# Kernel optimization log

Hardware: AMD Instinct MI355X
Metric: run time of the kernel (lower is better)

## Reference

```python
import jax, jax.numpy as jnp
import numpy as np

EPS = 1e-5
NEG_SLOPE = 0.2


def batchnorm_nodes(x, gamma, beta):
    # BatchNorm2d over channel=node axis; x: [N, T, D], stats over (T, D) per node
    m = x.mean(axis=(1, 2), keepdims=True)
    v = ((x - m) ** 2).mean(axis=(1, 2), keepdims=True)
    return (x - m) * jax.lax.rsqrt(v + EPS) * gamma[:, None, None] + beta[:, None, None]


def gat_relation(h, src, dst, W, al, ar, N):
    # h: [N, T, D]; W: [D, H, dh]; al/ar: [H, dh]
    z = jnp.einsum('ntd,dhe->nthe', h, W)              # [N, T, H, dh]
    el = jnp.einsum('nthe,he->nth', z, al)             # [N, T, H]
    er = jnp.einsum('nthe,he->nth', z, ar)
    e = jax.nn.leaky_relu(el[src] + er[dst], NEG_SLOPE)  # [E, T, H]
    emax = jax.ops.segment_max(e, dst, num_segments=N)   # [N, T, H]
    ex = jnp.exp(e - emax[dst])
    denom = jax.ops.segment_sum(ex, dst, num_segments=N)
    alpha = ex / jnp.maximum(denom[dst], 1e-16)          # segment softmax over in-edges
    msg = alpha[..., None] * z[src]                      # [E, T, H, dh]
    return jax.ops.segment_sum(msg, dst, num_segments=N)  # [N, T, H, dh]


def setup_inputs() -> dict:
    key = jax.random.key(0)
    ks = jax.random.split(key, 12)
    N, T, D, H, E, DFF = 10000, 12, 64, 4, 100000, 128
    dh = D // H
    s = 0.1
    return {
        'x': jax.random.normal(ks[0], (N, T, D), jnp.float32),
        'src1': jax.random.randint(ks[1], (E,), 0, N, jnp.int32),
        'dst1': jax.random.randint(ks[2], (E,), 0, N, jnp.int32),
        'src2': jax.random.randint(ks[3], (E,), 0, N, jnp.int32),
        'dst2': jax.random.randint(ks[4], (E,), 0, N, jnp.int32),
        'W1': jax.random.normal(ks[5], (D, H, dh), jnp.float32) * s,
        'al1': jax.random.normal(ks[6], (H, dh), jnp.float32) * s,
        'ar1': jax.random.normal(ks[7], (H, dh), jnp.float32) * s,
        'W2': jax.random.normal(ks[8], (D, H, dh), jnp.float32) * s,
        'al2': jax.random.normal(ks[9], (H, dh), jnp.float32) * s,
        'ar2': jax.random.normal(ks[10], (H, dh), jnp.float32) * s,
        'bn1_g': jnp.ones((N,), jnp.float32),
        'bn1_b': jnp.zeros((N,), jnp.float32),
        'bn2_g': jnp.ones((N,), jnp.float32),
        'bn2_b': jnp.zeros((N,), jnp.float32),
        'ff_w1': jax.random.normal(ks[11], (D, DFF), jnp.float32) * s,
        'ff_b1': jnp.zeros((DFF,), jnp.float32),
        'ff_w2': jax.random.normal(jax.random.fold_in(key, 99), (DFF, D), jnp.float32) * s,
        'ff_b2': jnp.zeros((D,), jnp.float32),
    }


def reference(x, src1, dst1, src2, dst2, W1, al1, ar1, W2, al2, ar2,
              bn1_g, bn1_b, bn2_g, bn2_b, ff_w1, ff_b1, ff_w2, ff_b2):
    N, T, D = x.shape
    h = batchnorm_nodes(x, bn1_g, bn1_b)
    # HeteroGraphConv: per-relation GAT, sum aggregation
    m = gat_relation(h, src1, dst1, W1, al1, ar1, N) \
      + gat_relation(h, src2, dst2, W2, al2, ar2, N)   # [N, T, H, dh]
    m = m.reshape(N, T, D)
    x2 = x + m                                          # residual (dropout=identity in eval)
    h2 = batchnorm_nodes(x2, bn2_g, bn2_b)
    ff = jax.nn.gelu(h2 @ ff_w1 + ff_b1, approximate=False) @ ff_w2 + ff_b2
    return x2 + ff
```

## Files before the change

kernel.cpp:

```cpp
#include <hip/hip_runtime.h>
#include <math.h>

constexpr int kT = 12;
constexpr float kNeg = 0.2f;
constexpr float kEps = 1e-5f;
constexpr float kLog2e = 1.44269504088896f;

typedef __attribute__((ext_vector_type(8))) short bf16x8;
typedef __attribute__((ext_vector_type(4))) float f32x4;
typedef __attribute__((ext_vector_type(2))) float f32x2;

__device__ __forceinline__ short f2bf(float f) {
  union { float f; unsigned u; } v;
  v.f = f;
  return (short)((v.u + 0x7fffu + ((v.u >> 16) & 1u)) >> 16);
}
__device__ __forceinline__ unsigned pack2(float a, float b) {
  return (unsigned)(unsigned short)f2bf(a) | ((unsigned)(unsigned short)f2bf(b) << 16);
}

__device__ __forceinline__ float wave_reduce_sum(float v) {
#pragma unroll
  for (int o = 32; o > 0; o >>= 1) v += __shfl_xor(v, o);
  return v;
}

template <int CTRL>
__device__ __forceinline__ float qperm(float v) {
  int i = __float_as_int(v);
  return __int_as_float(__builtin_amdgcn_update_dpp(i, i, CTRL, 0xf, 0xf, false));
}

__global__ void prep_kernel(const float* __restrict__ x, const float* __restrict__ g,
                            const float* __restrict__ b, float* __restrict__ scale,
                            float* __restrict__ shift, const float* __restrict__ fw1,
                            const float* __restrict__ fw2, const float* __restrict__ zW1,
                            const float* __restrict__ zW2, const float* __restrict__ al1,
                            const float* __restrict__ ar1, const float* __restrict__ al2,
                            const float* __restrict__ ar2, bf16x8* __restrict__ fw1f,
                            bf16x8* __restrict__ fw2f, bf16x8* __restrict__ zw1f,
                            bf16x8* __restrict__ zw2f, bf16x8* __restrict__ walf,
                            const int* __restrict__ dst1, const int* __restrict__ dst2,
                            int* __restrict__ deg1, int* __restrict__ deg2, int N, int E1,
                            int E2, int nBnBlk) {
  int blk = blockIdx.x;
  int lane = threadIdx.x & 63, wid = threadIdx.x >> 6;
  if (blk < nBnBlk) {
    int n = blk * 4 + wid;
    if (n < N) {
      const float* xr = x + (size_t)n * 768;
      float s = 0.f, s2 = 0.f;
#pragma unroll
      for (int c = 0; c < 3; c++) {
        float4 v = *(const float4*)&xr[c * 256 + lane * 4];
        s += v.x + v.y + v.z + v.w;
        s2 += v.x * v.x + v.y * v.y + v.z * v.z + v.w * v.w;
      }
      s = wave_reduce_sum(s);
      s2 = wave_reduce_sum(s2);
      if (lane == 0) {
        const float inv = 1.f / 768.f;
        float mean = s * inv;
        float var = s2 * inv - mean * mean;
        float sc = rsqrtf(var + kEps) * g[n];
        scale[n] = sc;
        shift[n] = b[n] - mean * sc;
      }
    }
    return;
  }
  blk -= nBnBlk;
  int m = lane & 15, q = lane >> 4;
  if (blk == 0) {
    for (int fi = wid; fi < 16; fi += 4) {
      int mt = fi >> 1, kc = fi & 1;
      bf16x8 v;
#pragma unroll
      for (int j = 0; j < 8; j++) v[j] = f2bf(fw1[(kc * 32 + q * 8 + j) * 128 + mt * 16 + m]);
      fw1f[fi * 64 + lane] = v;
    }
    return;
  }
  if (blk == 1) {
    for (int fi = wid; fi < 16; fi += 4) {
      int mt2 = fi >> 2, kc2 = fi & 3;
      bf16x8 u;
#pragma unroll
      for (int j = 0; j < 8; j++) u[j] = f2bf(fw2[(kc2 * 32 + q * 8 + j) * 64 + mt2 * 16 + m]);
      fw2f[fi * 64 + lane] = u;
    }
    return;
  }
  if (blk == 2) {
    for (int fi = wid; fi < 8; fi += 4) {
      int mt = fi >> 1, kc = fi & 1;
      bf16x8 v, u;
#pragma unroll
      for (int j = 0; j < 8; j++) {
        int d = kc * 32 + q * 8 + j;
        v[j] = f2bf(zW1[d * 64 + mt * 16 + m]);
        u[j] = f2bf(zW2[d * 64 + mt * 16 + m]);
      }
      zw1f[fi * 64 + lane] = v;
      zw2f[fi * 64 + lane] = u;
    }
    return;
  }
  if (blk == 3) {
    __shared__ float wal[16][64];
    for (int e0 = threadIdx.x; e0 < 1024; e0 += 256) {
      int f = e0 >> 6, d = e0 & 63;
      int h = f & 3;
      const float* av = (f < 4) ? al1 : (f < 8) ? ar1 : (f < 12) ? al2 : ar2;
      const float* W = (f < 8) ? zW1 : zW2;
      float s = 0.f;
#pragma unroll
      for (int e = 0; e < 16; e++) s += W[d * 64 + h * 16 + e] * av[h * 16 + e];
      wal[f][d] = s * kLog2e;
    }
    __syncthreads();
    if (wid == 0) {
#pragma unroll
      for (int kc = 0; kc < 2; kc++) {
        bf16x8 v;
#pragma unroll
        for (int j = 0; j < 8; j++) v[j] = f2bf(wal[m][kc * 32 + q * 8 + j]);
        walf[kc * 64 + lane] = v;
      }
    }
    return;
  }
  int i = (blk - 4) * 256 + threadIdx.x;
  if (i < E1) atomicAdd(&deg1[dst1[i]], 1);
  else if (i < E1 + E2) atomicAdd(&deg2[dst2[i - E1]], 1);
}

__global__ void scan_kernel(const int* __restrict__ deg1, int* __restrict__ off1,
                            const int* __restrict__ deg2, int* __restrict__ off2, int N) {
  const int* deg = blockIdx.x ? deg2 : deg1;
  int* off = blockIdx.x ? off2 : off1;
  __shared__ int wsum[16];
  __shared__ int carry;
  int tid = threadIdx.x, lane = tid & 63, wv = tid >> 6;
  if (tid == 0) { carry = 0; off[0] = 0; }
  __syncthreads();
  for (int base = 0; base < N; base += 1024) {
    int i = base + tid;
    int incl = (i < N) ? deg[i] : 0;
#pragma unroll
    for (int o = 1; o < 64; o <<= 1) {
      int y = __shfl_up(incl, o);
      if (lane >= o) incl += y;
    }
    if (lane == 63) wsum[wv] = incl;
    __syncthreads();
    if (tid < 16) {
      int p = wsum[tid];
#pragma unroll
      for (int o = 1; o < 16; o <<= 1) {
        int y = __shfl_up(p, o);
        if (tid >= o) p += y;
      }
      wsum[tid] = p;
    }
    __syncthreads();
    int prefix = carry + (wv > 0 ? wsum[wv - 1] : 0);
    if (i < N) off[i + 1] = prefix + incl;
    int total = carry + wsum[15];
    __syncthreads();
    if (tid == 0) carry = total;
    __syncthreads();
  }
}

__global__ __launch_bounds__(256) void fillzel_kernel(
    const int* __restrict__ src1, const int* __restrict__ dst1, const int* __restrict__ off1,
    int* __restrict__ cur1, int* __restrict__ scsr1, const int* __restrict__ src2,
    const int* __restrict__ dst2, const int* __restrict__ off2, int* __restrict__ cur2,
    int* __restrict__ scsr2, int E1, int E2, int nZelBlk,
    const float* __restrict__ x, const float* __restrict__ scale,
    const float* __restrict__ shift, const bf16x8* __restrict__ zw1f,
    const bf16x8* __restrict__ zw2f, const bf16x8* __restrict__ walf,
    unsigned short* __restrict__ z1, unsigned short* __restrict__ z2,
    float* __restrict__ el1, float* __restrict__ er1, float* __restrict__ el2,
    float* __restrict__ er2, int NT) {
  if ((int)blockIdx.x >= nZelBlk) {
    int i = ((int)blockIdx.x - nZelBlk) * 256 + threadIdx.x;
    if (i < E1) {
      int d = dst1[i];
      int p = atomicAdd(&cur1[d], 1);
      scsr1[off1[d] + p] = src1[i] * kT;
    } else if (i < E1 + E2) {
      int k = i - E1;
      int d = dst2[k];
      int p = atomicAdd(&cur2[d], 1);
      scsr2[off2[d] + p] = src2[k] * kT;
    }
    return;
  }
  __shared__ bf16x8 sW1[8][64];
  __shared__ bf16x8 sW2[8][64];
  __shared__ bf16x8 sWE[2][64];
  int lane = threadIdx.x & 63, wid = threadIdx.x >> 6;
  int m = lane & 15, q = lane >> 4;
  for (int fi = wid; fi < 8; fi += 4) {
    sW1[fi][lane] = zw1f[fi * 64 + lane];
    sW2[fi][lane] = zw2f[fi * 64 + lane];
  }
  if (wid == 0) {
    sWE[0][lane] = walf[lane];
    sWE[1][lane] = walf[64 + lane];
  }
  __syncthreads();
  int ntile = (NT + 15) / 16;
  for (int tile = blockIdx.x * 4 + wid; tile < ntile; tile += nZelBlk * 4) {
    int r0 = tile * 16;
    int row = r0 + m;
    int rowc = (row < NT) ? row : NT - 1;
    int n = rowc / kT;
    float sc = scale[n], sh = shift[n];
    bf16x8 hf[2];
#pragma unroll
    for (int kc = 0; kc < 2; kc++) {
      float4 p0 = *(const float4*)&x[(size_t)rowc * 64 + kc * 32 + q * 8];
      float4 p1 = *(const float4*)&x[(size_t)rowc * 64 + kc * 32 + q * 8 + 4];
      hf[kc][0] = f2bf(fmaf(p0.x, sc, sh));
      hf[kc][1] = f2bf(fmaf(p0.y, sc, sh));
      hf[kc][2] = f2bf(fmaf(p0.z, sc, sh));
      hf[kc][3] = f2bf(fmaf(p0.w, sc, sh));
      hf[kc][4] = f2bf(fmaf(p1.x, sc, sh));
      hf[kc][5] = f2bf(fmaf(p1.y, sc, sh));
      hf[kc][6] = f2bf(fmaf(p1.z, sc, sh));
      hf[kc][7] = f2bf(fmaf(p1.w, sc, sh));
    }
    f32x4 a1[4], a2[4], ae;
#pragma unroll
    for (int mt = 0; mt < 4; mt++) {
      a1[mt] = (f32x4){0.f, 0.f, 0.f, 0.f};
      a2[mt] = (f32x4){0.f, 0.f, 0.f, 0.f};
    }
    ae = (f32x4){0.f, 0.f, 0.f, 0.f};
#pragma unroll
    for (int kc = 0; kc < 2; kc++) {
#pragma unroll
      for (int mt = 0; mt < 4; mt++) {
        a1[mt] = __builtin_amdgcn_mfma_f32_16x16x32_bf16(sW1[mt * 2 + kc][lane], hf[kc],
                                                         a1[mt], 0, 0, 0);
        a2[mt] = __builtin_amdgcn_mfma_f32_16x16x32_bf16(sW2[mt * 2 + kc][lane], hf[kc],
                                                         a2[mt], 0, 0, 0);
      }
      ae = __builtin_amdgcn_mfma_f32_16x16x32_bf16(sWE[kc][lane], hf[kc], ae, 0, 0, 0);
    }
    if (row < NT) {
      float* edst = (q == 0) ? el1 : (q == 1) ? er1 : (q == 2) ? el2 : er2;
      *(float4*)&edst[(size_t)row * 4] = make_float4(ae[0], ae[1], ae[2], ae[3]);
#pragma unroll
      for (int mt = 0; mt < 4; mt++) {
        uint2 u1 = {pack2(a1[mt][0], a1[mt][1]), pack2(a1[mt][2], a1[mt][3])};
        uint2 u2 = {pack2(a2[mt][0], a2[mt][1]), pack2(a2[mt][2], a2[mt][3])};
        *(uint2*)&z1[(size_t)row * 64 + mt * 16 + 4 * q] = u1;
        *(uint2*)&z2[(size_t)row * 64 + mt * 16 + 4 * q] = u2;
      }
    }
  }
}

struct GBuf {
  uint2 z0, z1, z2, z3;
  float e;
};

__device__ __forceinline__ void pf_group(int sbl, int eb, int t, int zvoff,
                                         const float* __restrict__ elp,
                                         const unsigned short* __restrict__ zp, int qidx,
                                         GBuf& G) {
  int sg = __shfl(sbl, eb + qidx) + t;
  G.e = elp[(size_t)sg * 4];
  int s0 = __builtin_amdgcn_readlane(sbl, eb);
  int s1 = __builtin_amdgcn_readlane(sbl, eb + 1);
  int s2 = __builtin_amdgcn_readlane(sbl, eb + 2);
  int s3 = __builtin_amdgcn_readlane(sbl, eb + 3);
  G.z0 = *(const uint2*)(zp + (size_t)s0 * 64 + zvoff);
  G.z1 = *(const uint2*)(zp + (size_t)s1 * 64 + zvoff);
  G.z2 = *(const uint2*)(zp + (size_t)s2 * 64 + zvoff);
  G.z3 = *(const uint2*)(zp + (size_t)s3 * 64 + zvoff);
}

__device__ __forceinline__ void cg_group(const GBuf& G, float er_h, int rem, int qidx,
                                         float& den, f32x2& n01, f32x2& n23) {
  float ev = G.e + er_h;
  ev = fmaxf(ev, kNeg * ev);
  float w = exp2f(ev);
  w = (qidx < rem) ? w : 0.f;
  den += w;
  float w0 = qperm<0x00>(w);
  float w1 = qperm<0x55>(w);
  float w2 = qperm<0xAA>(w);
  float w3 = qperm<0xFF>(w);
  f32x2 v;
  v = (f32x2){__uint_as_float(G.z0.x << 16), __uint_as_float(G.z0.x & 0xffff0000u)};
  n01 += v * w0;
  v = (f32x2){__uint_as_float(G.z0.y << 16), __uint_as_float(G.z0.y & 0xffff0000u)};
  n23 += v * w0;
  v = (f32x2){__uint_as_float(G.z1.x << 16), __uint_as_float(G.z1.x & 0xffff0000u)};
  n01 += v * w1;
  v = (f32x2){__uint_as_float(G.z1.y << 16), __uint_as_float(G.z1.y & 0xffff0000u)};
  n23 += v * w1;
  v = (f32x2){__uint_as_float(G.z2.x << 16), __uint_as_float(G.z2.x & 0xffff0000u)};
  n01 += v * w2;
  v = (f32x2){__uint_as_float(G.z2.y << 16), __uint_as_float(G.z2.y & 0xffff0000u)};
  n23 += v * w2;
  v = (f32x2){__uint_as_float(G.z3.x << 16), __uint_as_float(G.z3.x & 0xffff0000u)};
  n01 += v * w3;
  v = (f32x2){__uint_as_float(G.z3.y << 16), __uint_as_float(G.z3.y & 0xffff0000u)};
  n23 += v * w3;
}

__device__ __forceinline__ void gat_rel(int n, int t, int zvoff, const int* __restrict__ scsr,
                                        const int* __restrict__ off,
                                        const float* __restrict__ elp, float er_h,
                                        const unsigned short* __restrict__ zp, int lane,
                                        int qidx, f32x2& a01, f32x2& a23) {
  int b0 = off[n], b1 = off[n + 1];
  if (b1 <= b0) return;
  float den = 0.f;
  f32x2 n01 = {0.f, 0.f}, n23 = {0.f, 0.f};
  for (int c0 = b0; c0 < b1; c0 += 64) {
    int cnt = b1 - c0;
    if (cnt > 64) cnt = 64;
    int idx = c0 + lane;
    int sbl = scsr[(idx < b1) ? idx : b1 - 1];
    GBuf A, B, C, D;
    pf_group(sbl, 0, t, zvoff, elp, zp, qidx, A);
    if (cnt > 4) pf_group(sbl, 4, t, zvoff, elp, zp, qidx, B);
    if (cnt > 8) pf_group(sbl, 8, t, zvoff, elp, zp, qidx, C);
    int g = 0;
    while (true) {
      if (g + 12 < cnt) pf_group(sbl, g + 12, t, zvoff, elp, zp, qidx, D);
      cg_group(A, er_h, cnt - g, qidx, den, n01, n23);
      g += 4;
      if (g >= cnt) break;
      if (g + 12 < cnt) pf_group(sbl, g + 12, t, zvoff, elp, zp, qidx, A);
      cg_group(B, er_h, cnt - g, qidx, den, n01, n23);
      g += 4;
      if (g >= cnt) break;
      if (g + 12 < cnt) pf_group(sbl, g + 12, t, zvoff, elp, zp, qidx, B);
      cg_group(C, er_h, cnt - g, qidx, den, n01, n23);
      g += 4;
      if (g >= cnt) break;
      if (g + 12 < cnt) pf_group(sbl, g + 12, t, zvoff, elp, zp, qidx, C);
      cg_group(D, er_h, cnt - g, qidx, den, n01, n23);
      g += 4;
      if (g >= cnt) break;
    }
  }
  den += qperm<0xB1>(den);
  den += qperm<0x4E>(den);
  float inv = 1.f / den;
  a01 += n01 * inv;
  a23 += n23 * inv;
}

__global__ __launch_bounds__(256) void agg_kernel(
    const float* __restrict__ x, const int* __restrict__ scsr1,
    const int* __restrict__ off1, const float* __restrict__ el1,
    const float* __restrict__ er1, const unsigned short* __restrict__ z1,
    const int* __restrict__ scsr2, const int* __restrict__ off2,
    const float* __restrict__ el2, const float* __restrict__ er2,
    const unsigned short* __restrict__ z2, float* __restrict__ x2,
    float* __restrict__ bn2s, float* __restrict__ bn2q, int N) {
  int wid = threadIdx.x >> 6, lane = threadIdx.x & 63;
  int w = blockIdx.x * 4 + wid;
  if (w >= N * 3) return;
  int n = w / 3;
  int t0 = (w - n * 3) * 4;
  int tl = lane >> 4, cg = lane & 15;
  int t = t0 + tl;
  int row = n * kT + t;
  int h = cg >> 2;
  int qidx = lane & 3;
  int zvoff = t * 64 + cg * 4;
  f32x2 a01 = {0.f, 0.f}, a23 = {0.f, 0.f};
  gat_rel(n, t, zvoff, scsr1, off1, el1 + h, er1[(size_t)row * 4 + h], z1, lane, qidx, a01,
          a23);
  gat_rel(n, t, zvoff, scsr2, off2, el2 + h, er2[(size_t)row * 4 + h], z2, lane, qidx, a01,
          a23);

  size_t base = (size_t)row * 64 + cg * 4;
  float4 xr = *(const float4*)&x[base];
  float4 o;
  o.x = xr.x + a01.x;
  o.y = xr.y + a01.y;
  o.z = xr.z + a23.x;
  o.w = xr.w + a23.y;
  *(float4*)&x2[base] = o;
  float s1 = o.x + o.y + o.z + o.w;
  float s2 = o.x * o.x + o.y * o.y + o.z * o.z + o.w * o.w;
  s1 = wave_reduce_sum(s1);
  s2 = wave_reduce_sum(s2);
  if (lane == 0) {
    atomicAdd(&bn2s[n], s1);
    atomicAdd(&bn2q[n], s2);
  }
}

__global__ __launch_bounds__(256, 2) void ff_kernel(
    const float* __restrict__ x2, const float* __restrict__ bn2s,
    const float* __restrict__ bn2q, const float* __restrict__ bng,
    const float* __restrict__ bnb, const bf16x8* __restrict__ w1f,
    const bf16x8* __restrict__ w2f, const float* __restrict__ b1,
    const float* __restrict__ b2, float* __restrict__ out, int NT) {
  __shared__ bf16x8 sW1[16][64];
  __shared__ bf16x8 sW2[16][64];
  __shared__ float sB1[128];
  __shared__ float sB2[64];
  int lane = threadIdx.x & 63, wid = threadIdx.x >> 6;
  int m = lane & 15, q = lane >> 4;
  {
    int fi0 = wid * 4;
#pragma unroll
    for (int k = 0; k < 4; k++) {
      sW1[fi0 + k][lane] = w1f[(fi0 + k) * 64 + lane];
      sW2[fi0 + k][lane] = w2f[(fi0 + k) * 64 + lane];
    }
    if (threadIdx.x < 128) sB1[threadIdx.x] = b1[threadIdx.x];
    if (threadIdx.x < 64) sB2[threadIdx.x] = b2[threadIdx.x];
  }
  __syncthreads();

  const float inv = 1.f / 768.f;
  int grp = blockIdx.x * 4 + wid;
  int ngrp = (NT + 31) / 32;
  if (grp >= ngrp) return;

  bf16x8 hf[2][2];
  f32x4 acc[2][8];
#pragma unroll
  for (int tt = 0; tt < 2; tt++) {
    int row = grp * 32 + tt * 16 + m;
    int rowc = (row < NT) ? row : NT - 1;
    int n = rowc / kT;
    float mean = bn2s[n] * inv;
    float var = bn2q[n] * inv - mean * mean;
    float sc = rsqrtf(var + kEps) * bng[n];
    float sh = bnb[n] - mean * sc;
#pragma unroll
    for (int kc = 0; kc < 2; kc++) {
      const float4 p0 = *(const float4*)&x2[(size_t)rowc * 64 + kc * 32 + q * 8];
      const float4 p1 = *(const float4*)&x2[(size_t)rowc * 64 + kc * 32 + q * 8 + 4];
      hf[tt][kc][0] = f2bf(fmaf(p0.x, sc, sh));
      hf[tt][kc][1] = f2bf(fmaf(p0.y, sc, sh));
      hf[tt][kc][2] = f2bf(fmaf(p0.z, sc, sh));
      hf[tt][kc][3] = f2bf(fmaf(p0.w, sc, sh));
      hf[tt][kc][4] = f2bf(fmaf(p1.x, sc, sh));
      hf[tt][kc][5] = f2bf(fmaf(p1.y, sc, sh));
      hf[tt][kc][6] = f2bf(fmaf(p1.z, sc, sh));
      hf[tt][kc][7] = f2bf(fmaf(p1.w, sc, sh));
    }
#pragma unroll
    for (int mt = 0; mt < 8; mt++) acc[tt][mt] = (f32x4){0.f, 0.f, 0.f, 0.f};
  }
#pragma unroll
  for (int kc = 0; kc < 2; kc++)
#pragma unroll
    for (int mt = 0; mt < 8; mt++)
#pragma unroll
      for (int tt = 0; tt < 2; tt++)
        acc[tt][mt] = __builtin_amdgcn_mfma_f32_16x16x32_bf16(sW1[mt * 2 + kc][lane],
                                                              hf[tt][kc], acc[tt][mt], 0, 0, 0);

  f32x4 acc2[2][4];
#pragma unroll
  for (int tt = 0; tt < 2; tt++)
#pragma unroll
    for (int mt = 0; mt < 4; mt++) acc2[tt][mt] = (f32x4){0.f, 0.f, 0.f, 0.f};
#pragma unroll
  for (int kc = 0; kc < 4; kc++) {
    float4 bb0 = *(const float4*)&sB1[(2 * kc) * 16 + 4 * q];
    float4 bb1 = *(const float4*)&sB1[(2 * kc + 1) * 16 + 4 * q];
    bf16x8 bf[2];
#pragma unroll
    for (int tt = 0; tt < 2; tt++) {
      float g0[4], g1[4];
      float u;
      u = acc[tt][2 * kc][0] + bb0.x; g0[0] = 0.5f * u * (1.f + erff(u * 0.70710678118654752f));
      u = acc[tt][2 * kc][1] + bb0.y; g0[1] = 0.5f * u * (1.f + erff(u * 0.70710678118654752f));
      u = acc[tt][2 * kc][2] + bb0.z; g0[2] = 0.5f * u * (1.f + erff(u * 0.70710678118654752f));
      u = acc[tt][2 * kc][3] + bb0.w; g0[3] = 0.5f * u * (1.f + erff(u * 0.70710678118654752f));
      u = acc[tt][2 * kc + 1][0] + bb1.x; g1[0] = 0.5f * u * (1.f + erff(u * 0.70710678118654752f));
      u = acc[tt][2 * kc + 1][1] + bb1.y; g1[1] = 0.5f * u * (1.f + erff(u * 0.70710678118654752f));
      u = acc[tt][2 * kc + 1][2] + bb1.z; g1[2] = 0.5f * u * (1.f + erff(u * 0.70710678118654752f));
      u = acc[tt][2 * kc + 1][3] + bb1.w; g1[3] = 0.5f * u * (1.f + erff(u * 0.70710678118654752f));
#pragma unroll
      for (int j = 0; j < 8; j++) {
        int srcq = (2 * q + (j >> 2)) & 3;
        int src = srcq * 16 + m;
        float v0 = __shfl(g0[j & 3], src);
        float v1 = __shfl(g1[j & 3], src);
        bf[tt][j] = f2bf((q >= 2) ? v1 : v0);
      }
    }
#pragma unroll
    for (int mt = 0; mt < 4; mt++)
#pragma unroll
      for (int tt = 0; tt < 2; tt++)
        acc2[tt][mt] = __builtin_amdgcn_mfma_f32_16x16x32_bf16(sW2[mt * 4 + kc][lane], bf[tt],
                                                               acc2[tt][mt], 0, 0, 0);
  }

#pragma unroll
  for (int tt = 0; tt < 2; tt++) {
    int row = grp * 32 + tt * 16 + m;
    if (row < NT) {
#pragma unroll
      for (int mt = 0; mt < 4; mt++) {
        size_t base = (size_t)row * 64 + mt * 16 + 4 * q;
        float4 xr = *(const float4*)&x2[base];
        float4 bb = *(const float4*)&sB2[mt * 16 + 4 * q];
        float4 o;
        o.x = acc2[tt][mt][0] + bb.x + xr.x;
        o.y = acc2[tt][mt][1] + bb.y + xr.y;
        o.z = acc2[tt][mt][2] + bb.z + xr.z;
        o.w = acc2[tt][mt][3] + bb.w + xr.w;
        *(float4*)&out[base] = o;
      }
    }
  }
}

extern "C" void kernel_launch(void* const* d_in, const int* in_sizes, int n_in,
                              void* d_out, int out_size, void* d_ws, size_t ws_size,
                              hipStream_t stream) {
  const float* x = (const float*)d_in[0];
  const int* src1 = (const int*)d_in[1];
  const int* dst1 = (const int*)d_in[2];
  const int* src2 = (const int*)d_in[3];
  const int* dst2 = (const int*)d_in[4];
  const float* W1 = (const float*)d_in[5];
  const float* al1 = (const float*)d_in[6];
  const float* ar1 = (const float*)d_in[7];
  const float* W2 = (const float*)d_in[8];
  const float* al2 = (const float*)d_in[9];
  const float* ar2 = (const float*)d_in[10];
  const float* g1 = (const float*)d_in[11];
  const float* b1 = (const float*)d_in[12];
  const float* g2 = (const float*)d_in[13];
  const float* b2 = (const float*)d_in[14];
  const float* fw1 = (const float*)d_in[15];
  const float* fb1 = (const float*)d_in[16];
  const float* fw2 = (const float*)d_in[17];
  const float* fb2 = (const float*)d_in[18];

  const int N = in_sizes[11];
  const int E1 = in_sizes[1];
  const int E2 = in_sizes[3];
  const int NT = N * kT;

  char* p = (char*)d_ws;
  auto alloc = [&](size_t bytes) -> char* {
    char* r = p;
    p += (bytes + 255) & ~(size_t)255;
    return r;
  };
  unsigned short* z1 = (unsigned short*)alloc((size_t)NT * 64 * 2);
  unsigned short* z2 = (unsigned short*)alloc((size_t)NT * 64 * 2);
  float* el1 = (float*)alloc((size_t)NT * 4 * 4);
  float* er1 = (float*)alloc((size_t)NT * 4 * 4);
  float* el2 = (float*)alloc((size_t)NT * 4 * 4);
  float* er2 = (float*)alloc((size_t)NT * 4 * 4);
  float* x2 = (float*)alloc((size_t)NT * 64 * 4);
  float* sc1 = (float*)alloc((size_t)N * 4);
  float* sh1 = (float*)alloc((size_t)N * 4);
  int* off1 = (int*)alloc((size_t)(N + 1) * 4);
  int* off2 = (int*)alloc((size_t)(N + 1) * 4);
  int* scsr1 = (int*)alloc((size_t)E1 * 4);
  int* scsr2 = (int*)alloc((size_t)E2 * 4);
  bf16x8* fw1f = (bf16x8*)alloc(16 * 64 * 16);
  bf16x8* fw2f = (bf16x8*)alloc(16 * 64 * 16);
  bf16x8* zw1f = (bf16x8*)alloc(8 * 64 * 16);
  bf16x8* zw2f = (bf16x8*)alloc(8 * 64 * 16);
  bf16x8* walf = (bf16x8*)alloc(2 * 64 * 16);
  char* zero_base = p;
  int* deg1 = (int*)alloc((size_t)N * 4);
  int* cur1 = (int*)alloc((size_t)N * 4);
  int* deg2 = (int*)alloc((size_t)N * 4);
  int* cur2 = (int*)alloc((size_t)N * 4);
  float* bn2s = (float*)alloc((size_t)N * 4);
  float* bn2q = (float*)alloc((size_t)N * 4);
  size_t zero_bytes = (size_t)(p - zero_base);
  hipMemsetAsync(zero_base, 0, zero_bytes, stream);

  const int nBnBlk = (N + 3) / 4;
  const int degBlk = (E1 + E2 + 255) / 256;
  prep_kernel<<<nBnBlk + 4 + degBlk, 256, 0, stream>>>(
      x, g1, b1, sc1, sh1, fw1, fw2, W1, W2, al1, ar1, al2, ar2, fw1f, fw2f, zw1f, zw2f, walf,
      dst1, dst2, deg1, deg2, N, E1, E2, nBnBlk);
  scan_kernel<<<2, 1024, 0, stream>>>(deg1, off1, deg2, off2, N);
  const int nZelBlk = 1875;
  fillzel_kernel<<<nZelBlk + degBlk, 256, 0, stream>>>(
      src1, dst1, off1, cur1, scsr1, src2, dst2, off2, cur2, scsr2, E1, E2, nZelBlk, x, sc1,
      sh1, zw1f, zw2f, walf, z1, z2, el1, er1, el2, er2, NT);
  agg_kernel<<<(N * 3 + 3) / 4, 256, 0, stream>>>(x, scsr1, off1, el1, er1, z1, scsr2, off2,
                                                  el2, er2, z2, x2, bn2s, bn2q, N);
  ff_kernel<<<((NT + 31) / 32 + 3) / 4, 256, 0, stream>>>(x2, bn2s, bn2q, g2, b2, fw1f, fw2f,
                                                          fb1, fb2, (float*)d_out, NT);
}
```

Before: 246.9 us.

## Replace serial CSR prefix scan with atomic-based per-wave segment allocation

The two-block serial scan over node degrees is replaced by a fully parallel kernel. Each wave scans its 64 degrees and reserves a contiguous range with one atomicAdd on a global counter. Offsets are no longer globally sorted, so the aggregation kernel now reads each node's end from off+deg instead of off[n+1]. This removes a long single-block latency step, at the cost of nondeterministic segment placement that may hurt locality slightly.

Result: faster. 241.9 us (-2.0%).

```diff
diff --git a/kernel.cpp b/kernel.cpp
--- a/kernel.cpp
+++ b/kernel.cpp
@@ -135,41 +135,30 @@
   else if (i < E1 + E2) atomicAdd(&deg2[dst2[i - E1]], 1);
 }
 
-__global__ void scan_kernel(const int* __restrict__ deg1, int* __restrict__ off1,
-                            const int* __restrict__ deg2, int* __restrict__ off2, int N) {
-  const int* deg = blockIdx.x ? deg2 : deg1;
-  int* off = blockIdx.x ? off2 : off1;
-  __shared__ int wsum[16];
-  __shared__ int carry;
-  int tid = threadIdx.x, lane = tid & 63, wv = tid >> 6;
-  if (tid == 0) { carry = 0; off[0] = 0; }
-  __syncthreads();
-  for (int base = 0; base < N; base += 1024) {
-    int i = base + tid;
-    int incl = (i < N) ? deg[i] : 0;
-#pragma unroll
-    for (int o = 1; o < 64; o <<= 1) {
-      int y = __shfl_up(incl, o);
-      if (lane >= o) incl += y;
-    }
-    if (lane == 63) wsum[wv] = incl;
-    __syncthreads();
-    if (tid < 16) {
-      int p = wsum[tid];
-#pragma unroll
-      for (int o = 1; o < 16; o <<= 1) {
-        int y = __shfl_up(p, o);
-        if (tid >= o) p += y;
-      }
-      wsum[tid] = p;
-    }
-    __syncthreads();
-    int prefix = carry + (wv > 0 ? wsum[wv - 1] : 0);
-    if (i < N) off[i + 1] = prefix + incl;
-    int total = carry + wsum[15];
-    __syncthreads();
-    if (tid == 0) carry = total;
-    __syncthreads();
+__global__ void alloc_kernel(const int* __restrict__ deg1, int* __restrict__ off1,
+                             int* __restrict__ ctr1, const int* __restrict__ deg2,
+                             int* __restrict__ off2, int* __restrict__ ctr2, int N) {
+  int n = blockIdx.x * 256 + threadIdx.x;
+  int lane = threadIdx.x & 63;
+  int d1 = (n < N) ? deg1[n] : 0;
+  int d2 = (n < N) ? deg2[n] : 0;
+  int i1 = d1, i2 = d2;
+#pragma unroll
+  for (int o = 1; o < 64; o <<= 1) {
+    int y1 = __shfl_up(i1, o), y2 = __shfl_up(i2, o);
+    if (lane >= o) { i1 += y1; i2 += y2; }
+  }
+  int tot1 = __shfl(i1, 63), tot2 = __shfl(i2, 63);
+  int base1 = 0, base2 = 0;
+  if (lane == 0) {
+    base1 = atomicAdd(ctr1, tot1);
+    base2 = atomicAdd(ctr2, tot2);
+  }
+  base1 = __shfl(base1, 0);
+  base2 = __shfl(base2, 0);
+  if (n < N) {
+    off1[n] = base1 + i1 - d1;
+    off2[n] = base2 + i2 - d2;
   }
 }
 
@@ -316,12 +305,11 @@
   n23 += v * w3;
 }
 
-__device__ __forceinline__ void gat_rel(int n, int t, int zvoff, const int* __restrict__ scsr,
-                                        const int* __restrict__ off,
+__device__ __forceinline__ void gat_rel(int b0, int b1, int t, int zvoff,
+                                        const int* __restrict__ scsr,
                                         const float* __restrict__ elp, float er_h,
                                         const unsigned short* __restrict__ zp, int lane,
                                         int qidx, f32x2& a01, f32x2& a23) {
-  int b0 = off[n], b1 = off[n + 1];
   if (b1 <= b0) return;
   float den = 0.f;
   f32x2 n01 = {0.f, 0.f}, n23 = {0.f, 0.f};
@@ -363,9 +351,10 @@
 
 __global__ __launch_bounds__(256) void agg_kernel(
     const float* __restrict__ x, const int* __restrict__ scsr1,
-    const int* __restrict__ off1, const float* __restrict__ el1,
-    const float* __restrict__ er1, const unsigned short* __restrict__ z1,
-    const int* __restrict__ scsr2, const int* __restrict__ off2,
+    const int* __restrict__ off1, const int* __restrict__ deg1,
+    const float* __restrict__ el1, const float* __restrict__ er1,
+    const unsigned short* __restrict__ z1, const int* __restrict__ scsr2,
+    const int* __restrict__ off2, const int* __restrict__ deg2,
     const float* __restrict__ el2, const float* __restrict__ er2,
     const unsigned short* __restrict__ z2, float* __restrict__ x2,
     float* __restrict__ bn2s, float* __restrict__ bn2q, int N) {
@@ -381,9 +370,11 @@
   int qidx = lane & 3;
   int zvoff = t * 64 + cg * 4;
   f32x2 a01 = {0.f, 0.f}, a23 = {0.f, 0.f};
-  gat_rel(n, t, zvoff, scsr1, off1, el1 + h, er1[(size_t)row * 4 + h], z1, lane, qidx, a01,
+  int b0a = off1[n], b1a = b0a + deg1[n];
+  int b0b = off2[n], b1b = b0b + deg2[n];
+  gat_rel(b0a, b1a, t, zvoff, scsr1, el1 + h, er1[(size_t)row * 4 + h], z1, lane, qidx, a01,
           a23);
-  gat_rel(n, t, zvoff, scsr2, off2, el2 + h, er2[(size_t)row * 4 + h], z2, lane, qidx, a01,
+  gat_rel(b0b, b1b, t, zvoff, scsr2, el2 + h, er2[(size_t)row * 4 + h], z2, lane, qidx, a01,
           a23);
 
   size_t base = (size_t)row * 64 + cg * 4;
@@ -587,6 +578,7 @@
   int* cur2 = (int*)alloc((size_t)N * 4);
   float* bn2s = (float*)alloc((size_t)N * 4);
   float* bn2q = (float*)alloc((size_t)N * 4);
+  int* ctrs = (int*)alloc(2 * 4);
   size_t zero_bytes = (size_t)(p - zero_base);
   hipMemsetAsync(zero_base, 0, zero_bytes, stream);
 
@@ -595,13 +587,14 @@
   prep_kernel<<<nBnBlk + 4 + degBlk, 256, 0, stream>>>(
       x, g1, b1, sc1, sh1, fw1, fw2, W1, W2, al1, ar1, al2, ar2, fw1f, fw2f, zw1f, zw2f, walf,
       dst1, dst2, deg1, deg2, N, E1, E2, nBnBlk);
-  scan_kernel<<<2, 1024, 0, stream>>>(deg1, off1, deg2, off2, N);
+  alloc_kernel<<<(N + 255) / 256, 256, 0, stream>>>(deg1, off1, &ctrs[0], deg2, off2,
+                                                    &ctrs[1], N);
   const int nZelBlk = 1875;
   fillzel_kernel<<<nZelBlk + degBlk, 256, 0, stream>>>(
       src1, dst1, off1, cur1, scsr1, src2, dst2, off2, cur2, scsr2, E1, E2, nZelBlk, x, sc1,
       sh1, zw1f, zw2f, walf, z1, z2, el1, er1, el2, er2, NT);
-  agg_kernel<<<(N * 3 + 3) / 4, 256, 0, stream>>>(x, scsr1, off1, el1, er1, z1, scsr2, off2,
-                                                  el2, er2, z2, x2, bn2s, bn2q, N);
+  agg_kernel<<<(N * 3 + 3) / 4, 256, 0, stream>>>(x, scsr1, off1, deg1, el1, er1, z1, scsr2,
+                                                  off2, deg2, el2, er2, z2, x2, bn2s, bn2q, N);
   ff_kernel<<<((NT + 31) / 32 + 3) / 4, 256, 0, stream>>>(x2, bn2s, bn2q, g2, b2, fw1f, fw2f,
                                                           fb1, fb2, (float*)d_out, NT);
 }
```
